# Kernel optimization log

Measured on AMD Instinct MI355X. Metric: run time of the kernel, lower is better.

The kernel has to match this reference:

```python
import jax, jax.numpy as jnp
import numpy as np

B, N, D, H, DA, DL = 8, 1024, 512, 8, 64, 64
DFF = 4 * D
EPS = 1e-6


def layer_norm(x, g, b):
    mu = jnp.mean(x, axis=-1, keepdims=True)
    var = jnp.mean(jnp.square(x - mu), axis=-1, keepdims=True)
    return (x - mu) * jax.lax.rsqrt(var + EPS) * g + b


def setup_inputs() -> dict:
    key = jax.random.key(0)
    ks = jax.random.split(key, 12)
    T = B * N
    x = jax.random.normal(ks[0], (T, D), dtype=jnp.float32)
    x_offsets = (jnp.arange(B + 1, dtype=jnp.int64) * N)
    invalid_attn_mask = jnp.tril(jnp.ones((N, N), dtype=jnp.float32))  # causal
    s = lambda fin: 1.0 / np.sqrt(fin)
    W_q = jax.random.normal(ks[1], (D, H * DA), jnp.float32) * s(D)
    b_q = jnp.zeros((H * DA,), jnp.float32)
    W_k = jax.random.normal(ks[2], (D, H * DA), jnp.float32) * s(D)
    b_k = jnp.zeros((H * DA,), jnp.float32)
    W_v = jax.random.normal(ks[3], (D, H * DL), jnp.float32) * s(D)
    b_v = jnp.zeros((H * DL,), jnp.float32)
    W_o = jax.random.normal(ks[4], (H * DL, D), jnp.float32) * s(H * DL)
    b_o = jnp.zeros((D,), jnp.float32)
    ln1_g = jnp.ones((D,), jnp.float32); ln1_b = jnp.zeros((D,), jnp.float32)
    ln2_g = jnp.ones((D,), jnp.float32); ln2_b = jnp.zeros((D,), jnp.float32)
    W_f1 = jax.random.normal(ks[5], (D, DFF), jnp.float32) * s(D)
    b_f1 = jnp.zeros((DFF,), jnp.float32)
    W_f2 = jax.random.normal(ks[6], (DFF, D), jnp.float32) * s(DFF)
    b_f2 = jnp.zeros((D,), jnp.float32)
    return dict(x=x, x_offsets=x_offsets, invalid_attn_mask=invalid_attn_mask,
                W_q=W_q, b_q=b_q, W_k=W_k, b_k=b_k, W_v=W_v, b_v=b_v,
                W_o=W_o, b_o=b_o, ln1_g=ln1_g, ln1_b=ln1_b, ln2_g=ln2_g,
                ln2_b=ln2_b, W_f1=W_f1, b_f1=b_f1, W_f2=W_f2, b_f2=b_f2)


def reference(x, x_offsets, invalid_attn_mask, W_q, b_q, W_k, b_k, W_v, b_v,
              W_o, b_o, ln1_g, ln1_b, ln2_g, ln2_b, W_f1, b_f1, W_f2, b_f2):
    T = x.shape[0]
    n = invalid_attn_mask.shape[-1]
    h = layer_norm(x, ln1_g, ln1_b)
    q = h @ W_q + b_q  # [T, H*DA]
    k = h @ W_k + b_k
    v = h @ W_v + b_v  # [T, H*DL]
    # jagged -> dense padding (vectorized)
    lengths = x_offsets[1:] - x_offsets[:-1]          # [B]
    pos = jnp.arange(n)
    idx = x_offsets[:-1, None] + pos[None, :]          # [B, n] flat token index
    valid = pos[None, :] < jnp.minimum(lengths, n)[:, None]
    idx_c = jnp.clip(idx, 0, T - 1)
    pq = jnp.where(valid[..., None], q[idx_c], 0.0).reshape(B, n, H, DA)
    pk = jnp.where(valid[..., None], k[idx_c], 0.0).reshape(B, n, H, DA)
    pv = jnp.where(valid[..., None], v[idx_c], 0.0).reshape(B, n, H, DL)
    scores = jnp.einsum('bnhd,bmhd->bhnm', pq, pk) / np.sqrt(DA)
    scores = jnp.where(invalid_attn_mask[None, None] == 0, -jnp.inf, scores)
    attn = jax.nn.softmax(scores, axis=-1)            # [B, H, n, n]
    out = jnp.einsum('bhnm,bmhd->bnhd', attn, pv).reshape(B, n, H * DL)
    # dense -> jagged unpadding (assumes all lengths <= n, as in setup)
    t = jnp.arange(T)
    b_idx = jnp.searchsorted(x_offsets, t, side='right') - 1
    p_idx = t - x_offsets[b_idx]
    attn_j = out[b_idx, p_idx]                         # [T, H*DL]
    x = x + (attn_j @ W_o + b_o)
    h2 = layer_norm(x, ln2_g, ln2_b)
    ffn = jax.nn.silu(h2 @ W_f1 + b_f1) @ W_f2 + b_f2
    return x + ffn
```

## Files before the change

### kernel.cpp

```cpp
#include <hip/hip_runtime.h>


typedef __bf16 bf16x8 __attribute__((ext_vector_type(8)));
typedef float f32x4 __attribute__((ext_vector_type(4)));

#define GLOAD16(g, l)                                                      \
  __builtin_amdgcn_global_load_lds(                                       \
      (const __attribute__((address_space(1))) void*)(g),                 \
      (__attribute__((address_space(3))) void*)(l), 16, 0, 0)

#define WAITVM(N) asm volatile("s_waitcnt vmcnt(" #N ")" ::: "memory")
#define WAITLGKM0 asm volatile("s_waitcnt lgkmcnt(0)" ::: "memory")
#define BAR() __builtin_amdgcn_s_barrier()

__global__ __launch_bounds__(256) void prep_kernel(
    const float* __restrict__ Wq, const float* __restrict__ Wk,
    const float* __restrict__ Wv, const float* __restrict__ Wo,
    const float* __restrict__ Wf1, const float* __restrict__ Wf2,
    const float* __restrict__ bq, const float* __restrict__ bk,
    const float* __restrict__ bv, __bf16* __restrict__ wqkv,
    __bf16* __restrict__ wo_t, __bf16* __restrict__ wf1_t,
    __bf16* __restrict__ wf2_t, float* __restrict__ bqkv) {
  __shared__ float t[32][33];
  const int id = blockIdx.x;
  if (id >= 3072) {
    int i = (id - 3072) * 256 + threadIdx.x;
    float v;
    if (i < 512) v = bq[i] * 0.125f;
    else if (i < 1024) v = bk[i - 512];
    else v = bv[i - 1024];
    bqkv[i] = v;
    return;
  }
  const float* src;
  __bf16* dst;
  int K, N, bx, by;
  float wscale = 1.0f;
  if (id < 1024) {
    const int which = id >> 8, tt = id & 255;
    bx = tt & 15;
    by = tt >> 4;
    K = 512;
    N = 512;
    if (which == 0) { src = Wq; dst = wqkv; wscale = 0.125f; }
    else if (which == 1) { src = Wk; dst = wqkv + 512 * 512; }
    else if (which == 2) { src = Wv; dst = wqkv + 1024 * 512; }
    else { src = Wo; dst = wo_t; }
  } else if (id < 2048) {
    const int tt = id - 1024;
    bx = tt & 63;
    by = tt >> 6;
    K = 512;
    N = 2048;
    src = Wf1;
    dst = wf1_t;
  } else {
    const int tt = id - 2048;
    bx = tt & 15;
    by = tt >> 4;
    K = 2048;
    N = 512;
    src = Wf2;
    dst = wf2_t;
  }
  const int n0 = bx * 32, k0 = by * 32;
  const int tx = threadIdx.x & 31, ty = threadIdx.x >> 5;
#pragma unroll
  for (int i = 0; i < 4; i++)
    t[ty + i * 8][tx] = src[(size_t)(k0 + ty + i * 8) * N + n0 + tx];
  __syncthreads();
#pragma unroll
  for (int i = 0; i < 4; i++)
    dst[(size_t)(n0 + ty + i * 8) * K + k0 + tx] =
        (__bf16)(t[tx][ty + i * 8] * wscale);
}

__global__ __launch_bounds__(256) void ln_kernel(const float* __restrict__ x,
                                                 const float* __restrict__ g,
                                                 const float* __restrict__ bta,
                                                 __bf16* __restrict__ out) {
  const int row = blockIdx.x * 4 + (threadIdx.x >> 6);
  const int lane = threadIdx.x & 63;
  const float4* xr = (const float4*)(x + (size_t)row * 512);
  float4 v0 = xr[lane * 2 + 0];
  float4 v1 = xr[lane * 2 + 1];
  float s = v0.x + v0.y + v0.z + v0.w + v1.x + v1.y + v1.z + v1.w;
  float sq = v0.x * v0.x + v0.y * v0.y + v0.z * v0.z + v0.w * v0.w +
             v1.x * v1.x + v1.y * v1.y + v1.z * v1.z + v1.w * v1.w;
#pragma unroll
  for (int o = 1; o < 64; o <<= 1) {
    s += __shfl_xor(s, o);
    sq += __shfl_xor(sq, o);
  }
  const float mu = s * (1.0f / 512.0f);
  const float var = sq * (1.0f / 512.0f) - mu * mu;
  const float rs = rsqrtf(var + 1e-6f);
  const float4* gr = (const float4*)g + lane * 2;
  const float4* br = (const float4*)bta + lane * 2;
  float4 g0 = gr[0], g1 = gr[1], b0 = br[0], b1 = br[1];
  bf16x8 o8;
  o8[0] = (__bf16)((v0.x - mu) * rs * g0.x + b0.x);
  o8[1] = (__bf16)((v0.y - mu) * rs * g0.y + b0.y);
  o8[2] = (__bf16)((v0.z - mu) * rs * g0.z + b0.z);
  o8[3] = (__bf16)((v0.w - mu) * rs * g0.w + b0.w);
  o8[4] = (__bf16)((v1.x - mu) * rs * g1.x + b1.x);
  o8[5] = (__bf16)((v1.y - mu) * rs * g1.y + b1.y);
  o8[6] = (__bf16)((v1.z - mu) * rs * g1.z + b1.z);
  o8[7] = (__bf16)((v1.w - mu) * rs * g1.w + b1.w);
  *(bf16x8*)(out + (size_t)row * 512 + lane * 8) = o8;
}

template <int EPI>
__global__ __launch_bounds__(256) void gemm_bt(
    const __bf16* __restrict__ A, const __bf16* __restrict__ Bt,
    const float* __restrict__ bias, const float* __restrict__ resid,
    void* __restrict__ outp, int M, int N, int K) {
  __shared__ __bf16 As[2][128 * 32];
  __shared__ __bf16 Bs[2][128 * 32];
  const int tid = threadIdx.x;
  const int lane = tid & 63;
  const int w = tid >> 6;
  const int brow = blockIdx.x * 128;
  const int bcol = blockIdx.y * 128;

  f32x4 acc[4][4] = {};

  const int srow = tid >> 2;
  const int sc = (tid & 3) ^ (srow & 3);
  const __bf16* a_src = A + (size_t)(brow + srow) * K + sc * 8;
  const __bf16* b_src = Bt + (size_t)(bcol + srow) * K + sc * 8;

  const int wr = w >> 1, wc = w & 1;
  const int lr = lane & 15, lg = lane >> 4;
  const int arow = wr * 64 + lr;
  const int brf = wc * 64 + lr;
  const int sw = ((lg ^ (lr & 3)) << 3);

#define STAGE128(buf, koff)                                                 \
  do {                                                                      \
    GLOAD16(a_src + (koff), &As[buf][w * 512]);                             \
    GLOAD16(a_src + (size_t)64 * K + (koff), &As[buf][2048 + w * 512]);     \
    GLOAD16(b_src + (koff), &Bs[buf][w * 512]);                             \
    GLOAD16(b_src + (size_t)64 * K + (koff), &Bs[buf][2048 + w * 512]);     \
  } while (0)

  const int T = K >> 5;
  STAGE128(0, 0);
  STAGE128(1, 32);

  for (int t = 0; t < T; ++t) {
    if (t + 1 < T) WAITVM(4);
    else WAITVM(0);
    BAR();
    const int cur = t & 1;
    bf16x8 af[4], bfv[4];
#pragma unroll
    for (int m = 0; m < 4; m++)
      af[m] = *(const bf16x8*)&As[cur][(arow + m * 16) * 32 + sw];
#pragma unroll
    for (int n = 0; n < 4; n++)
      bfv[n] = *(const bf16x8*)&Bs[cur][(brf + n * 16) * 32 + sw];
    WAITLGKM0;
    BAR();
    if (t + 2 < T) STAGE128(cur, (t + 2) * 32);
    __builtin_amdgcn_s_setprio(1);
#pragma unroll
    for (int m = 0; m < 4; m++)
#pragma unroll
      for (int n = 0; n < 4; n++)
        acc[m][n] =
            __builtin_amdgcn_mfma_f32_16x16x32_bf16(af[m], bfv[n], acc[m][n], 0, 0, 0);
    __builtin_amdgcn_s_setprio(0);
  }
#undef STAGE128

  const int rbase = brow + wr * 64 + (lg << 2);
  const int cbase = bcol + wc * 64 + lr;
#pragma unroll
  for (int m = 0; m < 4; m++) {
#pragma unroll
    for (int n = 0; n < 4; n++) {
      const int col = cbase + n * 16;
      const float bv = bias[col];
#pragma unroll
      for (int j = 0; j < 4; j++) {
        const int row = rbase + m * 16 + j;
        float v = acc[m][n][j] + bv;
        const size_t idx = (size_t)row * N + col;
        if (EPI == 0) {
          ((__bf16*)outp)[idx] = (__bf16)v;
        } else {
          ((__bf16*)outp)[idx] = (__bf16)(v / (1.0f + __expf(-v)));
        }
      }
    }
  }
}

template <int EPI>
__global__ __launch_bounds__(256) void gemm_bt_n64(
    const __bf16* __restrict__ A, const __bf16* __restrict__ Bt,
    const float* __restrict__ bias, const float* __restrict__ resid,
    void* __restrict__ outp, int M, int N, int K) {
  __shared__ __bf16 As[2][128 * 64];
  __shared__ __bf16 Bs[2][64 * 64];
  const int tid = threadIdx.x;
  const int lane = tid & 63;
  const int w = tid >> 6;
  const int brow = blockIdx.x * 128;
  const int bcol = blockIdx.y * 64;

  f32x4 acc[2][4] = {};

  const int srow = tid >> 3;
  const int sc = (tid & 7) ^ (srow & 7);
  const __bf16* a_src = A + (size_t)(brow + srow) * K + sc * 8;
  const __bf16* b_src = Bt + (size_t)(bcol + srow) * K + sc * 8;

  const int lr = lane & 15, lg = lane >> 4;
  const int arow0 = w * 32 + lr;
  const int sw0 = ((lg ^ (lr & 7)) << 3);

#define STAGE_N64(buf, koff)                                               \
  do {                                                                     \
    GLOAD16(a_src + (koff), &As[buf][w * 512]);                            \
    GLOAD16(a_src + (size_t)32 * K + (koff), &As[buf][2048 + w * 512]);    \
    GLOAD16(a_src + (size_t)64 * K + (koff), &As[buf][4096 + w * 512]);    \
    GLOAD16(a_src + (size_t)96 * K + (koff), &As[buf][6144 + w * 512]);    \
    GLOAD16(b_src + (koff), &Bs[buf][w * 512]);                            \
    GLOAD16(b_src + (size_t)32 * K + (koff), &Bs[buf][2048 + w * 512]);    \
  } while (0)

  const int T = K >> 6;
  STAGE_N64(0, 0);
  STAGE_N64(1, 64);

  for (int t = 0; t < T; ++t) {
    if (t + 1 < T) WAITVM(6);
    else WAITVM(0);
    BAR();
    const int cur = t & 1;
    bf16x8 af[2][2], bfv[4][2];
#pragma unroll
    for (int m = 0; m < 2; m++) {
      const int r = (arow0 + m * 16) * 64;
      af[m][0] = *(const bf16x8*)&As[cur][r + sw0];
      af[m][1] = *(const bf16x8*)&As[cur][r + (sw0 ^ 32)];
    }
#pragma unroll
    for (int n = 0; n < 4; n++) {
      const int r = (n * 16 + lr) * 64;
      bfv[n][0] = *(const bf16x8*)&Bs[cur][r + sw0];
      bfv[n][1] = *(const bf16x8*)&Bs[cur][r + (sw0 ^ 32)];
    }
    WAITLGKM0;
    BAR();
    if (t + 2 < T) STAGE_N64(cur, (t + 2) * 64);
    __builtin_amdgcn_s_setprio(1);
#pragma unroll
    for (int m = 0; m < 2; m++)
#pragma unroll
      for (int n = 0; n < 4; n++)
#pragma unroll
        for (int s = 0; s < 2; s++)
          acc[m][n] = __builtin_amdgcn_mfma_f32_16x16x32_bf16(
              af[m][s], bfv[n][s], acc[m][n], 0, 0, 0);
    __builtin_amdgcn_s_setprio(0);
  }
#undef STAGE_N64

  const int rbase = brow + w * 32 + (lg << 2);
  const int cbase = bcol + lr;
#pragma unroll
  for (int m = 0; m < 2; m++) {
#pragma unroll
    for (int n = 0; n < 4; n++) {
      const int col = cbase + n * 16;
      const float bv = bias[col];
#pragma unroll
      for (int j = 0; j < 4; j++) {
        const int row = rbase + m * 16 + j;
        float v = acc[m][n][j] + bv;
        const size_t idx = (size_t)row * N + col;
        if (EPI == 2) {
          ((float*)outp)[idx] = v + resid[idx];
        } else {
          ((float*)outp)[idx] += v;
        }
      }
    }
  }
}

__global__ __launch_bounds__(256) void vtrans_kernel(
    const __bf16* __restrict__ qkv, __bf16* __restrict__ vt) {
  const int bh = blockIdx.y, b = bh >> 3, h = bh & 7;
  const int n0 = blockIdx.x * 64;
  __shared__ __bf16 t[64][72];
  const int tx = threadIdx.x & 3, ty = threadIdx.x >> 2;
  const __bf16* src =
      qkv + (size_t)(b * 1024 + n0 + ty) * 1536 + 1024 + h * 64 + tx * 16;
  bf16x8 v0 = *(const bf16x8*)(src);
  bf16x8 v1 = *(const bf16x8*)(src + 8);
  *(bf16x8*)&t[ty][tx * 16] = v0;
  *(bf16x8*)&t[ty][tx * 16 + 8] = v1;
  __syncthreads();
  bf16x8 o0, o1;
#pragma unroll
  for (int j = 0; j < 8; j++) {
    o0[j] = t[tx * 16 + j][ty];
    o1[j] = t[tx * 16 + 8 + j][ty];
  }
  __bf16* dst = vt + (size_t)(bh * 64 + ty) * 1024 + n0 + tx * 16;
  *(bf16x8*)dst = o0;
  *(bf16x8*)(dst + 8) = o1;
}

__global__ __launch_bounds__(256) void attn_kernel(
    const __bf16* __restrict__ qkv, const __bf16* __restrict__ vt,
    __bf16* __restrict__ out) {
  const int bid = blockIdx.x;
  const int qb = 15 - (bid >> 6);
  const int bh = bid & 63;
  const int b = bh >> 3, h = bh & 7;
  const int tid = threadIdx.x;
  const int lane = tid & 63, w = tid >> 6;
  const int qr = qb * 64 + w * 16;
  const int lr = lane & 15, lg = lane >> 4;

  __shared__ __bf16 Ks[2][64 * 64];
  __shared__ __bf16 Vs[2][64 * 64];
  __shared__ __bf16 Plds[4][16][72];

  const __bf16* Qp = qkv + (size_t)b * 1024 * 1536 + h * 64;
  const __bf16* Kp = Qp + 512;
  const __bf16* Vp = vt + (size_t)bh * 64 * 1024;

  const int srow = tid >> 3;
  const int kc = (tid & 7) ^ (srow & 7);
  const __bf16* ksrcA = Kp + (size_t)srow * 1536 + kc * 8;
  const __bf16* ksrcB = Kp + (size_t)(srow + 32) * 1536 + kc * 8;
  const __bf16* vsrcA = Vp + (size_t)srow * 1024 + kc * 8;
  const __bf16* vsrcB = Vp + (size_t)(srow + 32) * 1024 + kc * 8;

#define STAGE_ATT(buf, nb)                                                 \
  do {                                                                     \
    GLOAD16(ksrcA + (size_t)(nb) * 1536, &Ks[buf][w * 512]);               \
    GLOAD16(ksrcB + (size_t)(nb) * 1536, &Ks[buf][2048 + w * 512]);        \
    GLOAD16(vsrcA + (nb), &Vs[buf][w * 512]);                              \
    GLOAD16(vsrcB + (nb), &Vs[buf][2048 + w * 512]);                       \
  } while (0)

  bf16x8 qf[2];
#pragma unroll
  for (int s = 0; s < 2; s++)
    qf[s] = *(const bf16x8*)(Qp + (size_t)(qr + lr) * 1536 + s * 32 + lg * 8);

  f32x4 accO[4] = {};
  float l_run[4] = {0.f, 0.f, 0.f, 0.f};

  STAGE_ATT(0, 0);
  if (qb >= 1) STAGE_ATT(1, 64);

  for (int kt = 0; kt <= qb; ++kt) {
    const int kb = kt * 64;
    const int cur = kt & 1;
    if (kt < qb) WAITVM(4);
    else WAITVM(0);
    BAR();
    f32x4 sa[4] = {};
    __builtin_amdgcn_s_setprio(1);
#pragma unroll
    for (int n = 0; n < 4; n++) {
      const int row = n * 16 + lr;
#pragma unroll
      for (int s = 0; s < 2; s++) {
        bf16x8 kf = *(const bf16x8*)&Ks[cur][row * 64 +
                                             (((s * 4 + lg) ^ (row & 7)) << 3)];
        sa[n] = __builtin_amdgcn_mfma_f32_16x16x32_bf16(qf[s], kf, sa[n], 0, 0, 0);
      }
    }
    __builtin_amdgcn_s_setprio(0);
    const bool domask = (kt == qb);
#pragma unroll
    for (int j = 0; j < 4; j++) {
      const int row = qr + lg * 4 + j;
#pragma unroll
      for (int n = 0; n < 4; n++) {
        float p = __expf(sa[n][j]);
        if (domask && (kb + n * 16 + lr) > row) p = 0.f;
        sa[n][j] = p;
        l_run[j] += p;
      }
    }
#pragma unroll
    for (int n = 0; n < 4; n++)
#pragma unroll
      for (int j = 0; j < 4; j++)
        Plds[w][lg * 4 + j][n * 16 + lr] = (__bf16)sa[n][j];
    __builtin_amdgcn_s_setprio(1);
#pragma unroll
    for (int s = 0; s < 2; s++) {
      bf16x8 pf = *(const bf16x8*)&Plds[w][lr][s * 32 + lg * 8];
#pragma unroll
      for (int n = 0; n < 4; n++) {
        const int row = n * 16 + lr;
        bf16x8 vf = *(const bf16x8*)&Vs[cur][row * 64 +
                                             (((s * 4 + lg) ^ (row & 7)) << 3)];
        accO[n] = __builtin_amdgcn_mfma_f32_16x16x32_bf16(pf, vf, accO[n], 0, 0, 0);
      }
    }
    __builtin_amdgcn_s_setprio(0);
    WAITLGKM0;
    BAR();
    if (kt + 2 <= qb) STAGE_ATT(cur, (kt + 2) * 64);
  }
#undef STAGE_ATT

#pragma unroll
  for (int j = 0; j < 4; j++) {
#pragma unroll
    for (int o = 1; o < 16; o <<= 1) l_run[j] += __shfl_xor(l_run[j], o);
  }
#pragma unroll
  for (int n = 0; n < 4; n++) {
#pragma unroll
    for (int j = 0; j < 4; j++) {
      const int row = qr + lg * 4 + j;
      const float v = accO[n][j] / l_run[j];
      out[(size_t)(b * 1024 + row) * 512 + h * 64 + n * 16 + lr] = (__bf16)v;
    }
  }
}

extern "C" void kernel_launch(void* const* d_in, const int* in_sizes, int n_in,
                              void* d_out, int out_size, void* d_ws,
                              size_t ws_size, hipStream_t stream) {
  const float* x = (const float*)d_in[0];
  const float* Wq = (const float*)d_in[3];
  const float* bq = (const float*)d_in[4];
  const float* Wk = (const float*)d_in[5];
  const float* bk = (const float*)d_in[6];
  const float* Wv = (const float*)d_in[7];
  const float* bv = (const float*)d_in[8];
  const float* Wo = (const float*)d_in[9];
  const float* bo = (const float*)d_in[10];
  const float* ln1g = (const float*)d_in[11];
  const float* ln1b = (const float*)d_in[12];
  const float* ln2g = (const float*)d_in[13];
  const float* ln2b = (const float*)d_in[14];
  const float* Wf1 = (const float*)d_in[15];
  const float* bf1 = (const float*)d_in[16];
  const float* Wf2 = (const float*)d_in[17];
  const float* bf2 = (const float*)d_in[18];
  float* out = (float*)d_out;

  char* ws = (char*)d_ws;
  if (ws_size < 65018880ULL) return;
  __bf16* h1 = (__bf16*)(ws + 0);
  __bf16* h2 = (__bf16*)(ws + 8388608);
  __bf16* attn = (__bf16*)(ws + 16777216);
  __bf16* wqkv = (__bf16*)(ws + 25165824);
  __bf16* wo_t = (__bf16*)(ws + 26738688);
  __bf16* wf1_t = (__bf16*)(ws + 27262976);
  __bf16* wf2_t = (__bf16*)(ws + 29360128);
  float* bqkv = (float*)(ws + 31457280);
  __bf16* qkv = (__bf16*)(ws + 31464448);
  __bf16* vt = (__bf16*)(ws + 56630272);
  __bf16* ffn1 = qkv;

  prep_kernel<<<3078, 256, 0, stream>>>(Wq, Wk, Wv, Wo, Wf1, Wf2, bq, bk, bv,
                                        wqkv, wo_t, wf1_t, wf2_t, bqkv);

  ln_kernel<<<2048, 256, 0, stream>>>(x, ln1g, ln1b, h1);
  gemm_bt<0><<<dim3(64, 12), 256, 0, stream>>>(h1, wqkv, bqkv, nullptr, qkv,
                                               8192, 1536, 512);
  vtrans_kernel<<<dim3(16, 64), 256, 0, stream>>>(qkv, vt);
  attn_kernel<<<1024, 256, 0, stream>>>(qkv, vt, attn);
  gemm_bt_n64<2><<<dim3(64, 8), 256, 0, stream>>>(attn, wo_t, bo, x, out, 8192,
                                                  512, 512);
  ln_kernel<<<2048, 256, 0, stream>>>(out, ln2g, ln2b, h2);
  gemm_bt<1><<<dim3(64, 16), 256, 0, stream>>>(h2, wf1_t, bf1, nullptr, ffn1,
                                               8192, 2048, 512);
  gemm_bt_n64<3><<<dim3(64, 8), 256, 0, stream>>>(ffn1, wf2_t, bf2, nullptr,
                                                  out, 8192, 512, 2048);
}
```

Measured before the change: 137.9 us.

## Double attention query tile to 128 rows per block to reuse K/V tiles

Each attention block now covers 128 query rows (32 per wave, as two 16-row MFMA sub-tiles) instead of 64, so every staged K/V tile in LDS feeds twice as many MFMAs. The grid is halved to 512 blocks and the causal mask now applies to the last two key tiles. The aim is to halve K/V global-to-LDS traffic and barrier overhead per unit of work. The cost is higher register pressure, fewer blocks to spread over the CUs, and coarser causal load balance.

```diff
diff --git a/kernel.cpp b/kernel.cpp
--- a/kernel.cpp
+++ b/kernel.cpp
@@ -320,17 +320,17 @@
     const __bf16* __restrict__ qkv, const __bf16* __restrict__ vt,
     __bf16* __restrict__ out) {
   const int bid = blockIdx.x;
-  const int qb = 15 - (bid >> 6);
+  const int qb = 7 - (bid >> 6);
   const int bh = bid & 63;
   const int b = bh >> 3, h = bh & 7;
   const int tid = threadIdx.x;
   const int lane = tid & 63, w = tid >> 6;
-  const int qr = qb * 64 + w * 16;
+  const int qr = qb * 128 + w * 32;
   const int lr = lane & 15, lg = lane >> 4;
 
   __shared__ __bf16 Ks[2][64 * 64];
   __shared__ __bf16 Vs[2][64 * 64];
-  __shared__ __bf16 Plds[4][16][72];
+  __shared__ __bf16 Plds[4][32][72];
 
   const __bf16* Qp = qkv + (size_t)b * 1024 * 1536 + h * 64;
   const __bf16* Kp = Qp + 512;
@@ -351,24 +351,27 @@
     GLOAD16(vsrcB + (nb), &Vs[buf][2048 + w * 512]);                       \
   } while (0)
 
-  bf16x8 qf[2];
-#pragma unroll
-  for (int s = 0; s < 2; s++)
-    qf[s] = *(const bf16x8*)(Qp + (size_t)(qr + lr) * 1536 + s * 32 + lg * 8);
-
-  f32x4 accO[4] = {};
-  float l_run[4] = {0.f, 0.f, 0.f, 0.f};
-
+  bf16x8 qf[2][2];
+#pragma unroll
+  for (int m = 0; m < 2; m++)
+#pragma unroll
+    for (int s = 0; s < 2; s++)
+      qf[m][s] = *(const bf16x8*)(Qp + (size_t)(qr + m * 16 + lr) * 1536 +
+                                  s * 32 + lg * 8);
+
+  f32x4 accO[2][4] = {};
+  float l_run[2][4] = {};
+
+  const int NT = 2 * qb + 2;
   STAGE_ATT(0, 0);
-  if (qb >= 1) STAGE_ATT(1, 64);
-
-  for (int kt = 0; kt <= qb; ++kt) {
-    const int kb = kt * 64;
+  if (NT > 1) STAGE_ATT(1, 64);
+
+  for (int kt = 0; kt < NT; ++kt) {
     const int cur = kt & 1;
-    if (kt < qb) WAITVM(4);
+    if (kt + 1 < NT) WAITVM(4);
     else WAITVM(0);
     BAR();
-    f32x4 sa[4] = {};
+    f32x4 sa[2][4] = {};
     __builtin_amdgcn_s_setprio(1);
 #pragma unroll
     for (int n = 0; n < 4; n++) {
@@ -377,58 +380,74 @@
       for (int s = 0; s < 2; s++) {
         bf16x8 kf = *(const bf16x8*)&Ks[cur][row * 64 +
                                              (((s * 4 + lg) ^ (row & 7)) << 3)];
-        sa[n] = __builtin_amdgcn_mfma_f32_16x16x32_bf16(qf[s], kf, sa[n], 0, 0, 0);
+#pragma unroll
+        for (int m = 0; m < 2; m++)
+          sa[m][n] =
+              __builtin_amdgcn_mfma_f32_16x16x32_bf16(qf[m][s], kf, sa[m][n], 0, 0, 0);
       }
     }
     __builtin_amdgcn_s_setprio(0);
-    const bool domask = (kt == qb);
-#pragma unroll
-    for (int j = 0; j < 4; j++) {
-      const int row = qr + lg * 4 + j;
-#pragma unroll
-      for (int n = 0; n < 4; n++) {
-        float p = __expf(sa[n][j]);
-        if (domask && (kb + n * 16 + lr) > row) p = 0.f;
-        sa[n][j] = p;
-        l_run[j] += p;
+    const bool domask = (kt >= 2 * qb);
+#pragma unroll
+    for (int m = 0; m < 2; m++) {
+#pragma unroll
+      for (int j = 0; j < 4; j++) {
+        const int row = qr + m * 16 + lg * 4 + j;
+#pragma unroll
+        for (int n = 0; n < 4; n++) {
+          float p = __expf(sa[m][n][j]);
+          if (domask && (kt * 64 + n * 16 + lr) > row) p = 0.f;
+          sa[m][n][j] = p;
+          l_run[m][j] += p;
+        }
       }
     }
 #pragma unroll
-    for (int n = 0; n < 4; n++)
-#pragma unroll
-      for (int j = 0; j < 4; j++)
-        Plds[w][lg * 4 + j][n * 16 + lr] = (__bf16)sa[n][j];
+    for (int m = 0; m < 2; m++)
+#pragma unroll
+      for (int n = 0; n < 4; n++)
+#pragma unroll
+        for (int j = 0; j < 4; j++)
+          Plds[w][m * 16 + lg * 4 + j][n * 16 + lr] = (__bf16)sa[m][n][j];
     __builtin_amdgcn_s_setprio(1);
 #pragma unroll
     for (int s = 0; s < 2; s++) {
-      bf16x8 pf = *(const bf16x8*)&Plds[w][lr][s * 32 + lg * 8];
+      bf16x8 pf0 = *(const bf16x8*)&Plds[w][lr][s * 32 + lg * 8];
+      bf16x8 pf1 = *(const bf16x8*)&Plds[w][16 + lr][s * 32 + lg * 8];
 #pragma unroll
       for (int n = 0; n < 4; n++) {
         const int row = n * 16 + lr;
         bf16x8 vf = *(const bf16x8*)&Vs[cur][row * 64 +
                                              (((s * 4 + lg) ^ (row & 7)) << 3)];
-        accO[n] = __builtin_amdgcn_mfma_f32_16x16x32_bf16(pf, vf, accO[n], 0, 0, 0);
+        accO[0][n] = __builtin_amdgcn_mfma_f32_16x16x32_bf16(pf0, vf, accO[0][n], 0, 0, 0);
+        accO[1][n] = __builtin_amdgcn_mfma_f32_16x16x32_bf16(pf1, vf, accO[1][n], 0, 0, 0);
       }
     }
     __builtin_amdgcn_s_setprio(0);
     WAITLGKM0;
     BAR();
-    if (kt + 2 <= qb) STAGE_ATT(cur, (kt + 2) * 64);
+    if (kt + 2 < NT) STAGE_ATT(cur, (kt + 2) * 64);
   }
 #undef STAGE_ATT
 
 #pragma unroll
-  for (int j = 0; j < 4; j++) {
-#pragma unroll
-    for (int o = 1; o < 16; o <<= 1) l_run[j] += __shfl_xor(l_run[j], o);
-  }
-#pragma unroll
-  for (int n = 0; n < 4; n++) {
+  for (int m = 0; m < 2; m++)
 #pragma unroll
     for (int j = 0; j < 4; j++) {
-      const int row = qr + lg * 4 + j;
-      const float v = accO[n][j] / l_run[j];
-      out[(size_t)(b * 1024 + row) * 512 + h * 64 + n * 16 + lr] = (__bf16)v;
+#pragma unroll
+      for (int o = 1; o < 16; o <<= 1)
+        l_run[m][j] += __shfl_xor(l_run[m][j], o);
+    }
+#pragma unroll
+  for (int m = 0; m < 2; m++) {
+#pragma unroll
+    for (int n = 0; n < 4; n++) {
+#pragma unroll
+      for (int j = 0; j < 4; j++) {
+        const int row = qr + m * 16 + lg * 4 + j;
+        const float v = accO[m][n][j] / l_run[m][j];
+        out[(size_t)(b * 1024 + row) * 512 + h * 64 + n * 16 + lr] = (__bf16)v;
+      }
     }
   }
 }
@@ -476,7 +495,7 @@
   gemm_bt<0><<<dim3(64, 12), 256, 0, stream>>>(h1, wqkv, bqkv, nullptr, qkv,
                                                8192, 1536, 512);
   vtrans_kernel<<<dim3(16, 64), 256, 0, stream>>>(qkv, vt);
-  attn_kernel<<<1024, 256, 0, stream>>>(qkv, vt, attn);
+  attn_kernel<<<512, 256, 0, stream>>>(qkv, vt, attn);
   gemm_bt_n64<2><<<dim3(64, 8), 256, 0, stream>>>(attn, wo_t, bo, x, out, 8192,
                                                   512, 512);
   ln_kernel<<<2048, 256, 0, stream>>>(out, ln2g, ln2b, h2);
```

After: 146.4 us. 6.2% more time.
